# Optimization experiments

Measured on AMD Instinct MI355X. Metric: run time of the kernel, lower is better.

## Reference

```python
import jax, jax.numpy as jnp
import numpy as np

B, N_TOKENS, D, K = 16, 4096, 256, 4096
COMMITMENT_COST = 0.25


def setup_inputs() -> dict:
    key = jax.random.key(0)
    k1, k2 = jax.random.split(key)
    x = jax.random.normal(k1, (B, N_TOKENS, D), dtype=jnp.float32)
    # nn.Embedding init uniform(-1/K, 1/K); scale is irrelevant to correctness,
    # use the same distribution for fidelity.
    codebook = jax.random.uniform(k2, (K, D), dtype=jnp.float32,
                                  minval=-1.0 / K, maxval=1.0 / K)
    return {"x": x, "codebook": codebook}


def reference(x, codebook):
    Bb, Nn, Dd = x.shape
    x_flat = x.reshape(-1, Dd)                                    # [BN, D]
    dist_sq = (jnp.sum(x_flat * x_flat, axis=1, keepdims=True)
               + jnp.sum(codebook * codebook, axis=1)
               - 2.0 * x_flat @ codebook.T)                       # [BN, K]
    dist_sq = jnp.maximum(dist_sq, 0.0)
    idx = jnp.argmin(dist_sq, axis=1)                             # [BN]
    q_flat = codebook[idx]                                        # [BN, D]
    q = q_flat.reshape(x.shape)

    x_sg = jax.lax.stop_gradient(x_flat)
    q_sg = jax.lax.stop_gradient(q_flat)
    codebook_loss = jnp.mean((q_flat - x_sg) ** 2, axis=-1).reshape(Bb, Nn)
    commit_loss = jnp.mean((x_flat - q_sg) ** 2, axis=-1).reshape(Bb, Nn)
    per_token_loss = codebook_loss + COMMITMENT_COST * commit_loss
    mean_vq_loss = jnp.mean(per_token_loss)

    q_st = x + jax.lax.stop_gradient(q - x)                       # straight-through

    counts = jnp.zeros((codebook.shape[0],), dtype=jnp.float32).at[idx].add(1.0)
    avg_probs = counts / x_flat.shape[0]
    perplexity = jnp.exp(-jnp.sum(avg_probs * jnp.log(avg_probs + 1e-10)))

    return q_st, mean_vq_loss, perplexity, idx
```

## Files before the change

### kernel.cpp

```cpp
#include <hip/hip_runtime.h>
#include <hip/hip_bf16.h>
#include <cstdint>
#include <cstddef>

#define D 256
#define NTOK 65536
#define KCODES 4096
#define Q_ELEMS (NTOK * D)
#define DELTA 3.0e-4f
#define CAP 24

typedef short bf16x8 __attribute__((ext_vector_type(8)));
typedef float f32x4 __attribute__((ext_vector_type(4)));
typedef unsigned short ushort8 __attribute__((ext_vector_type(8)));

__device__ __forceinline__ void gload_lds16(const float* g, float* l) {
  __builtin_amdgcn_global_load_lds(
      (const __attribute__((address_space(1))) void*)(g),
      (__attribute__((address_space(3))) void*)(l), 16, 0, 0);
}
__device__ __forceinline__ unsigned short f2bf(float f) {
  __hip_bfloat16 h = __float2bfloat16(f);
  unsigned short u;
  __builtin_memcpy(&u, &h, 2);
  return u;
}

__global__ __launch_bounds__(256) void ee_kernel(const float* __restrict__ cb,
                                                 float* __restrict__ se) {
  const int row = blockIdx.x * 4 + (threadIdx.x >> 6);
  const int lane = threadIdx.x & 63;
  const float4 v = reinterpret_cast<const float4*>(cb + (size_t)row * D)[lane];
  double s = (double)v.x * v.x + (double)v.y * v.y +
             (double)v.z * v.z + (double)v.w * v.w;
#pragma unroll
  for (int o = 32; o > 0; o >>= 1) s += __shfl_down(s, o, 64);
  if (lane == 0) se[row] = (float)s;
}

__global__ __launch_bounds__(256) void xx_kernel(const float* __restrict__ x,
                                                 float* __restrict__ sx) {
  const int row = blockIdx.x * 4 + (threadIdx.x >> 6);
  const int lane = threadIdx.x & 63;
  const float4 v = reinterpret_cast<const float4*>(x + (size_t)row * D)[lane];
  double s = (double)v.x * v.x + (double)v.y * v.y +
             (double)v.z * v.z + (double)v.w * v.w;
#pragma unroll
  for (int o = 32; o > 0; o >>= 1) s += __shfl_down(s, o, 64);
  if (lane == 0) sx[row] = (float)s;
}

__global__ __launch_bounds__(256) void pack_e_kernel(const float* __restrict__ cb,
                                                     unsigned short* __restrict__ bpack) {
  const int gid = blockIdx.x * 256 + threadIdx.x;
  const int c = gid >> 2;
  const int kt = gid & 3;
  const int row = c & 127;
  const int swz = (row & 7) << 3;
  unsigned short* dst = bpack + ((size_t)((c >> 7) * 4 + kt)) * 8192 + row * 64;
  const float* src = cb + (size_t)c * D + kt * 64;
#pragma unroll
  for (int j = 0; j < 8; ++j) {
    ushort8 o;
#pragma unroll
    for (int e = 0; e < 8; ++e) o[e] = f2bf(src[j * 8 + e]);
    *reinterpret_cast<ushort8*>(dst + ((j * 8) ^ swz)) = o;
  }
}

__global__ __launch_bounds__(512, 1) void screen2_kernel(
    const float* __restrict__ x, const unsigned short* __restrict__ bpack,
    const float* __restrict__ se, unsigned int* __restrict__ ccnt_g,
    int* __restrict__ cand_g, float* __restrict__ cval_g,
    float* __restrict__ rm_g) {
  __shared__ __attribute__((aligned(16))) unsigned short bbuf[5][8192];
  __shared__ float se_lds[KCODES];
  __shared__ int cand[256][CAP];
  __shared__ float cval[256][CAP];
  __shared__ unsigned int ccnt[256];

  const int tid = threadIdx.x;
  const int lane = tid & 63;
  const int w = tid >> 6;
  const int l15 = lane & 15;
  const int kg = lane >> 4;
  const int tok0 = blockIdx.x * 256;

  if (tid < 256) ccnt[tid] = 0;
  {
    const float4* s4 = reinterpret_cast<const float4*>(se);
    float4* d4 = reinterpret_cast<float4*>(se_lds);
    d4[tid * 2 + 0] = s4[tid * 2 + 0];
    d4[tid * 2 + 1] = s4[tid * 2 + 1];
  }

  bf16x8 ah[2][8];
#pragma unroll
  for (int gi = 0; gi < 2; ++gi) {
    const int t = tok0 + w * 32 + gi * 16 + l15;
    const float* xp = x + (size_t)t * D;
#pragma unroll
    for (int ks = 0; ks < 8; ++ks) {
      const float4 v0 = *reinterpret_cast<const float4*>(xp + ks * 32 + kg * 8);
      const float4 v1 = *reinterpret_cast<const float4*>(xp + ks * 32 + kg * 8 + 4);
      const float xv[8] = {v0.x, v0.y, v0.z, v0.w, v1.x, v1.y, v1.z, v1.w};
      bf16x8 h;
#pragma unroll
      for (int e = 0; e < 8; ++e) h[e] = (short)f2bf(xv[e]);
      ah[gi][ks] = h;
    }
  }

  auto STAGE = [&](int u) {
    const char* s = (const char*)bpack + (size_t)u * 16384 + w * 2048 + lane * 16;
    char* d = (char*)&bbuf[u % 5][0] + w * 2048;
    gload_lds16((const float*)s, (float*)d);
    gload_lds16((const float*)(s + 1024), (float*)(d + 1024));
  };

  asm volatile("s_waitcnt vmcnt(0)" ::: "memory");
  STAGE(0); STAGE(1); STAGE(2); STAGE(3);
  asm volatile("s_waitcnt vmcnt(6) lgkmcnt(0)" ::: "memory");
  __builtin_amdgcn_s_barrier();
  __builtin_amdgcn_sched_barrier(0);

  float rm[2][4];
#pragma unroll
  for (int fr = 0; fr < 2; ++fr)
#pragma unroll
    for (int q = 0; q < 4; ++q) rm[fr][q] = 3.4e38f;

  f32x4 acc[2][8];

  for (int ct4 = 0; ct4 < 32; ++ct4) {
#pragma unroll
    for (int kt = 0; kt < 4; ++kt) {
      const int u = ct4 * 4 + kt;
      if (u + 4 < 128) STAGE(u + 4);
      if (kt == 0) {
#pragma unroll
        for (int fr = 0; fr < 2; ++fr)
#pragma unroll
          for (int fc = 0; fc < 8; ++fc) acc[fr][fc] = (f32x4){0.f, 0.f, 0.f, 0.f};
      }
      const unsigned short* bb = &bbuf[u % 5][0];
#pragma unroll
      for (int kh = 0; kh < 2; ++kh) {
        const int ks = kt * 2 + kh;
        bf16x8 bfrag[8];
#pragma unroll
        for (int fc = 0; fc < 8; ++fc) {
          const int row = fc * 16 + l15;
          const int off = row * 64 + ((kh * 32 + kg * 8) ^ ((row & 7) << 3));
          bfrag[fc] = *reinterpret_cast<const bf16x8*>(bb + off);
        }
#pragma unroll
        for (int fr = 0; fr < 2; ++fr)
#pragma unroll
          for (int fc = 0; fc < 8; ++fc)
            acc[fr][fc] = __builtin_amdgcn_mfma_f32_16x16x32_bf16(
                ah[fr][ks], bfrag[fc], acc[fr][fc], 0, 0, 0);
      }
      if (kt == 3) {
        float sef[8];
#pragma unroll
        for (int fc = 0; fc < 8; ++fc)
          sef[fc] = se_lds[ct4 * 128 + fc * 16 + l15];
#pragma unroll
        for (int fr = 0; fr < 2; ++fr)
#pragma unroll
          for (int q = 0; q < 4; ++q) {
            float m = fmaf(-2.0f, acc[fr][0][q], sef[0]);
#pragma unroll
            for (int fc = 1; fc < 8; ++fc)
              m = fminf(m, fmaf(-2.0f, acc[fr][fc][q], sef[fc]));
            m = fminf(m, __shfl_xor(m, 1, 64));
            m = fminf(m, __shfl_xor(m, 2, 64));
            m = fminf(m, __shfl_xor(m, 4, 64));
            m = fminf(m, __shfl_xor(m, 8, 64));
            rm[fr][q] = fminf(rm[fr][q], m);
            const float thr = rm[fr][q] + DELTA;
            const int tl = w * 32 + fr * 16 + kg * 4 + q;
#pragma unroll
            for (int fc = 0; fc < 8; ++fc) {
              const float s = fmaf(-2.0f, acc[fr][fc][q], sef[fc]);
              if (s <= thr) {
                const unsigned p = atomicAdd(&ccnt[tl], 1u);
                if (p < CAP) {
                  cand[tl][p] = ct4 * 128 + fc * 16 + l15;
                  cval[tl][p] = s;
                }
              }
            }
          }
      }
      if (u != 127) {
        if (u <= 123) asm volatile("s_waitcnt vmcnt(6)" ::: "memory");
        else          asm volatile("s_waitcnt vmcnt(0)" ::: "memory");
        __builtin_amdgcn_s_barrier();
        __builtin_amdgcn_sched_barrier(0);
      }
    }
  }

  __syncthreads();
  if (tid < 256) ccnt_g[tok0 + tid] = ccnt[tid];
  if (l15 == 0) {
#pragma unroll
    for (int fr = 0; fr < 2; ++fr)
#pragma unroll
      for (int q = 0; q < 4; ++q)
        rm_g[tok0 + w * 32 + fr * 16 + kg * 4 + q] = rm[fr][q];
  }
  for (int j = tid; j < 256 * CAP; j += 512) {
    const int tk = j / CAP;
    const int p = j - tk * CAP;
    cand_g[(size_t)(tok0 + tk) * CAP + p] = cand[tk][p];
    cval_g[(size_t)(tok0 + tk) * CAP + p] = cval[tk][p];
  }
}

__global__ __launch_bounds__(256) void rescore_kernel(
    const float* __restrict__ x, const float* __restrict__ cb,
    const float* __restrict__ se, const float* __restrict__ sx,
    const unsigned int* __restrict__ ccnt_g, const int* __restrict__ cand_g,
    const float* __restrict__ cval_g, const float* __restrict__ rm_g,
    int* __restrict__ idx_i, float* __restrict__ idxf_out,
    unsigned int* __restrict__ ovf_count, int* __restrict__ ovf_list) {
  const int t = blockIdx.x * 256 + threadIdx.x;
  const unsigned n = ccnt_g[t];
  if (n > CAP) {
    const unsigned p = atomicAdd(ovf_count, 1u);
    ovf_list[p] = t;
    return;
  }
  const float thr = rm_g[t] + DELTA;
  const float sxv = sx[t];
  const float4* xp = reinterpret_cast<const float4*>(x + (size_t)t * D);
  float bq = 3.4e38f;
  int bc = 0x7fffffff;
  for (unsigned k = 0; k < n; ++k) {
    if (cval_g[(size_t)t * CAP + k] > thr) continue;
    const int c = cand_g[(size_t)t * CAP + k];
    const float4* cp = reinterpret_cast<const float4*>(cb + (size_t)c * D);
    float acc = 0.0f;
#pragma unroll 8
    for (int d4 = 0; d4 < 64; ++d4) {
      const float4 xv = xp[d4];
      const float4 ev = cp[d4];
      acc = fmaf(xv.x, ev.x, acc);
      acc = fmaf(xv.y, ev.y, acc);
      acc = fmaf(xv.z, ev.z, acc);
      acc = fmaf(xv.w, ev.w, acc);
    }
    const float r = sxv + se[c];
    const float q = r - 2.0f * acc;
    if (q < bq || (q == bq && c < bc)) { bq = q; bc = c; }
  }
  idx_i[t] = bc;
  idxf_out[t] = (float)bc;
}

__global__ __launch_bounds__(256) void ovf_kernel(
    const float* __restrict__ x, const float* __restrict__ cb,
    const float* __restrict__ se, const float* __restrict__ sx,
    const unsigned int* __restrict__ ovf_count, const int* __restrict__ ovf_list,
    int* __restrict__ idx_i, float* __restrict__ idxf_out) {
  __shared__ float bvv[256];
  __shared__ int bii[256];
  const int tid = threadIdx.x;
  const unsigned cnt = *ovf_count;
  for (unsigned i = blockIdx.x; i < cnt; i += gridDim.x) {
    const int t = ovf_list[i];
    const float sxv = sx[t];
    const float4* xp = reinterpret_cast<const float4*>(x + (size_t)t * D);
    float bq = 3.4e38f;
    int bc = 0x7fffffff;
    for (int c = tid; c < KCODES; c += 256) {
      const float4* cp = reinterpret_cast<const float4*>(cb + (size_t)c * D);
      float acc = 0.0f;
#pragma unroll 8
      for (int d4 = 0; d4 < 64; ++d4) {
        const float4 xv = xp[d4];
        const float4 ev = cp[d4];
        acc = fmaf(xv.x, ev.x, acc);
        acc = fmaf(xv.y, ev.y, acc);
        acc = fmaf(xv.z, ev.z, acc);
        acc = fmaf(xv.w, ev.w, acc);
      }
      const float r = sxv + se[c];
      const float q = r - 2.0f * acc;
      if (q < bq || (q == bq && c < bc)) { bq = q; bc = c; }
    }
    bvv[tid] = bq;
    bii[tid] = bc;
    __syncthreads();
    for (int o = 128; o > 0; o >>= 1) {
      if (tid < o) {
        const float v2 = bvv[tid + o];
        const int c2 = bii[tid + o];
        if (v2 < bvv[tid] || (v2 == bvv[tid] && c2 < bii[tid])) {
          bvv[tid] = v2;
          bii[tid] = c2;
        }
      }
      __syncthreads();
    }
    if (tid == 0) {
      idx_i[t] = bii[0];
      idxf_out[t] = (float)bii[0];
    }
    __syncthreads();
  }
}

__global__ __launch_bounds__(256) void argmin_fb_kernel(const float* __restrict__ x,
                                                        const float* __restrict__ cb,
                                                        const float* __restrict__ se,
                                                        const float* __restrict__ sx,
                                                        int* __restrict__ idx_out,
                                                        float* __restrict__ idxf_out) {
  __shared__ __attribute__((aligned(16))) float xs[64 * 128];
  __shared__ __attribute__((aligned(16))) float es[64 * 128];
  const int tid = threadIdx.x;
  const int lane = tid & 63;
  const int w = tid >> 6;
  const int wt = w & 1;
  const int wc = w >> 1;
  const int tgl = lane & 7;
  const int cgl = lane >> 3;
  const int t0 = wt * 64 + tgl * 8;
  const int c0 = wc * 64 + cgl * 8;
  const int tok0 = blockIdx.x * 128;
  float sxf[8];
#pragma unroll
  for (int i = 0; i < 8; ++i) sxf[i] = sx[tok0 + t0 + i];
  float bv[8];
  int bi[8];
#pragma unroll
  for (int i = 0; i < 8; ++i) { bv[i] = 3.4e38f; bi[i] = 0; }
  for (int ct = 0; ct < KCODES / 128; ++ct) {
    float acc[8][8] = {};
    for (int kt = 0; kt < 4; ++kt) {
      __syncthreads();
      {
        const float* xsrc = x + (size_t)tok0 * D + kt * 64;
        const float* esrc = cb + (size_t)(ct * 128) * D + kt * 64;
#pragma unroll
        for (int p = 0; p < 8; ++p) {
          const int idx = p * 256 + tid;
          const int t = idx >> 4;
          const int c = idx & 15;
          const int colp = (t + 8 * (c >> 1)) & 127;
          const float4 xv = *reinterpret_cast<const float4*>(xsrc + (size_t)t * D + c * 4);
          float* xd = &xs[(c * 4) * 128 + colp];
          xd[0] = xv.x; xd[128] = xv.y; xd[256] = xv.z; xd[384] = xv.w;
          const float4 ev = *reinterpret_cast<const float4*>(esrc + (size_t)t * D + c * 4);
          float* ed = &es[(c * 4) * 128 + colp];
          ed[0] = ev.x; ed[128] = ev.y; ed[256] = ev.z; ed[384] = ev.w;
        }
      }
      __syncthreads();
      for (int kp = 0; kp < 8; ++kp) {
        const float* xb = &xs[(kp * 8) * 128 + ((t0 + 8 * kp) & 127)];
        const float* eb = &es[(kp * 8) * 128 + ((c0 + 8 * kp) & 127)];
#pragma unroll
        for (int k2 = 0; k2 < 8; ++k2) {
          const float4 xv0 = *reinterpret_cast<const float4*>(xb + k2 * 128);
          const float4 xv1 = *reinterpret_cast<const float4*>(xb + k2 * 128 + 4);
          const float4 ev0 = *reinterpret_cast<const float4*>(eb + k2 * 128);
          const float4 ev1 = *reinterpret_cast<const float4*>(eb + k2 * 128 + 4);
          const float xa[8] = {xv0.x, xv0.y, xv0.z, xv0.w, xv1.x, xv1.y, xv1.z, xv1.w};
          const float ea[8] = {ev0.x, ev0.y, ev0.z, ev0.w, ev1.x, ev1.y, ev1.z, ev1.w};
#pragma unroll
          for (int i = 0; i < 8; ++i)
#pragma unroll
            for (int j = 0; j < 8; ++j) acc[i][j] = fmaf(xa[i], ea[j], acc[i][j]);
        }
      }
    }
#pragma unroll
    for (int j = 0; j < 8; ++j) {
      const int cidx = ct * 128 + c0 + j;
      const float sef = se[cidx];
#pragma unroll
      for (int i = 0; i < 8; ++i) {
        const float r = sxf[i] + sef;
        const float s = r - 2.0f * acc[i][j];
        if (s < bv[i]) { bv[i] = s; bi[i] = cidx; }
      }
    }
  }
  __syncthreads();
  float* red_val = xs;
  int* red_idx = reinterpret_cast<int*>(xs + 128 * 17);
  const int g = wc * 8 + cgl;
#pragma unroll
  for (int i = 0; i < 8; ++i) {
    red_val[(t0 + i) * 17 + g] = bv[i];
    red_idx[(t0 + i) * 17 + g] = bi[i];
  }
  __syncthreads();
  if (tid < 128) {
    float v = red_val[tid * 17 + 0];
    int ix = red_idx[tid * 17 + 0];
#pragma unroll
    for (int gg = 1; gg < 16; ++gg) {
      const float vv = red_val[tid * 17 + gg];
      const int ii = red_idx[tid * 17 + gg];
      if (vv < v || (vv == v && ii < ix)) { v = vv; ix = ii; }
    }
    idx_out[tok0 + tid] = ix;
    idxf_out[tok0 + tid] = (float)ix;
  }
}

__global__ __launch_bounds__(256) void finalize_kernel(const float* __restrict__ x,
                                                       const float* __restrict__ cb,
                                                       const int* __restrict__ idx,
                                                       float* __restrict__ q_out,
                                                       unsigned int* __restrict__ counts,
                                                       double* __restrict__ partials) {
  __shared__ double tok_s[16];
  const int tid = threadIdx.x;
  const int lt = tid >> 4;
  const int ld = tid & 15;
  const int t = blockIdx.x * 16 + lt;
  const int id = idx[t];
  const float* xp = x + (size_t)t * D + ld * 16;
  const float* ep = cb + (size_t)id * D + ld * 16;
  float* qp = q_out + (size_t)t * D + ld * 16;
  float s = 0.0f;
#pragma unroll
  for (int c = 0; c < 4; ++c) {
    const float4 xv = reinterpret_cast<const float4*>(xp)[c];
    const float4 ev = reinterpret_cast<const float4*>(ep)[c];
    const float d0 = ev.x - xv.x, d1 = ev.y - xv.y;
    const float d2 = ev.z - xv.z, d3 = ev.w - xv.w;
    s = fmaf(d0, d0, s);
    s = fmaf(d1, d1, s);
    s = fmaf(d2, d2, s);
    s = fmaf(d3, d3, s);
    float4 qv;
    qv.x = xv.x + d0;
    qv.y = xv.y + d1;
    qv.z = xv.z + d2;
    qv.w = xv.w + d3;
    reinterpret_cast<float4*>(qp)[c] = qv;
  }
#pragma unroll
  for (int o = 8; o > 0; o >>= 1) s += __shfl_down(s, o, 16);
  if (ld == 0) {
    atomicAdd(&counts[id], 1u);
    tok_s[lt] = (double)s;
  }
  __syncthreads();
  if (tid == 0) {
    double bs = 0.0;
    for (int i = 0; i < 16; ++i) bs += tok_s[i];
    partials[blockIdx.x] = bs;
  }
}

__global__ __launch_bounds__(256) void final_kernel(const unsigned int* __restrict__ counts,
                                                    const double* __restrict__ partials,
                                                    float* __restrict__ loss_out,
                                                    float* __restrict__ perp_out) {
  __shared__ double sh[256];
  const int tid = threadIdx.x;
  double ls = 0.0;
  for (int i = tid; i < NTOK / 16; i += 256) ls += partials[i];
  sh[tid] = ls;
  __syncthreads();
#pragma unroll
  for (int o = 128; o > 0; o >>= 1) {
    if (tid < o) sh[tid] += sh[tid + o];
    __syncthreads();
  }
  if (tid == 0) {
    *loss_out = (float)(sh[0] * (1.25 / (256.0 * 65536.0)));
  }
  __syncthreads();
  double hs = 0.0;
  for (int i = tid; i < KCODES; i += 256) {
    const float p = (float)counts[i] / 65536.0f;
    hs += (double)(p * logf(p + 1e-10f));
  }
  sh[tid] = hs;
  __syncthreads();
#pragma unroll
  for (int o = 128; o > 0; o >>= 1) {
    if (tid < o) sh[tid] += sh[tid + o];
    __syncthreads();
  }
  if (tid == 0) *perp_out = expf((float)(-sh[0]));
}

extern "C" void kernel_launch(void* const* d_in, const int* in_sizes, int n_in,
                              void* d_out, int out_size, void* d_ws, size_t ws_size,
                              hipStream_t stream) {
  (void)in_sizes; (void)n_in; (void)out_size;
  const float* x = (const float*)d_in[0];
  const float* cb = (const float*)d_in[1];

  float* out = (float*)d_out;
  float* q_out = out;
  float* loss_out = out + (size_t)Q_ELEMS;
  float* perp_out = out + (size_t)Q_ELEMS + 1;
  float* idxf_out = out + (size_t)Q_ELEMS + 2;

  char* ws = (char*)d_ws;
  float* se = (float*)(ws + 0);
  unsigned int* counts = (unsigned int*)(ws + (16 << 10));
  double* partials = (double*)(ws + (32 << 10));
  int* idx_i = (int*)(ws + (64 << 10));
  float* sx = (float*)(ws + (320 << 10));
  unsigned int* ovf_count = (unsigned int*)(ws + (576 << 10));
  int* ovf_list = (int*)(ws + (580 << 10));
  unsigned int* ccnt_g = (unsigned int*)(ws + (1 << 20));
  float* rm_g = (float*)(ws + (3 << 19));
  int* cand_g = (int*)(ws + (2 << 20));
  float* cval_g = (float*)(ws + (8 << 20));
  unsigned short* bpack = (unsigned short*)(ws + (14 << 20));

  hipMemsetAsync(counts, 0, KCODES * sizeof(unsigned int), stream);
  hipMemsetAsync(ovf_count, 0, sizeof(unsigned int), stream);
  ee_kernel<<<KCODES / 4, 256, 0, stream>>>(cb, se);
  xx_kernel<<<NTOK / 4, 256, 0, stream>>>(x, sx);

  if (ws_size >= (size_t)20 * 1024 * 1024) {
    pack_e_kernel<<<64, 256, 0, stream>>>(cb, bpack);
    screen2_kernel<<<NTOK / 256, 512, 0, stream>>>(x, bpack, se, ccnt_g, cand_g,
                                                   cval_g, rm_g);
    rescore_kernel<<<NTOK / 256, 256, 0, stream>>>(x, cb, se, sx, ccnt_g, cand_g,
                                                   cval_g, rm_g, idx_i, idxf_out,
                                                   ovf_count, ovf_list);
    ovf_kernel<<<64, 256, 0, stream>>>(x, cb, se, sx, ovf_count, ovf_list,
                                       idx_i, idxf_out);
  } else {
    argmin_fb_kernel<<<NTOK / 128, 256, 0, stream>>>(x, cb, se, sx, idx_i, idxf_out);
  }
  finalize_kernel<<<NTOK / 16, 256, 0, stream>>>(x, cb, idx_i, q_out, counts, partials);
  final_kernel<<<1, 256, 0, stream>>>(counts, partials, loss_out, perp_out);
}
```

Before: 396.5 us.

## Fuse rescore with finalize, pack candidates, shrink screen blocks for two-per-CU occupancy

The screening kernel now uses 256-thread blocks over 128 tokens with a 3-deep LDS ring, so two blocks can share a CU. Codebook norms are held in LDS as bf16, and each candidate's score and index are packed into a single 32-bit word, with the cap lowered to 16. The rescore kernel now also computes ||x||^2, gathers q, writes the straight-through output and accumulates loss and counts, which removes the separate xx and finalize passes over x. Risks: lower-precision candidate scores and norms, more overflow tokens from the smaller cap, and a full barrier after every k-step in place of the previous finer-grained waits.

```diff
diff --git a/kernel.cpp b/kernel.cpp
--- a/kernel.cpp
+++ b/kernel.cpp
@@ -8,7 +8,7 @@
 #define KCODES 4096
 #define Q_ELEMS (NTOK * D)
 #define DELTA 3.0e-4f
-#define CAP 24
+#define CAP 16
 
 typedef short bf16x8 __attribute__((ext_vector_type(8)));
 typedef float f32x4 __attribute__((ext_vector_type(4)));
@@ -24,6 +24,11 @@
   unsigned short u;
   __builtin_memcpy(&u, &h, 2);
   return u;
+}
+__device__ __forceinline__ float bf2f(unsigned short u) {
+  __hip_bfloat16 h;
+  __builtin_memcpy(&h, &u, 2);
+  return __bfloat162float(h);
 }
 
 __global__ __launch_bounds__(256) void ee_kernel(const float* __restrict__ cb,
@@ -68,30 +73,33 @@
   }
 }
 
-__global__ __launch_bounds__(512, 1) void screen2_kernel(
+__global__ __launch_bounds__(256, 2) void screen3_kernel(
     const float* __restrict__ x, const unsigned short* __restrict__ bpack,
     const float* __restrict__ se, unsigned int* __restrict__ ccnt_g,
-    int* __restrict__ cand_g, float* __restrict__ cval_g,
-    float* __restrict__ rm_g) {
-  __shared__ __attribute__((aligned(16))) unsigned short bbuf[5][8192];
-  __shared__ float se_lds[KCODES];
-  __shared__ int cand[256][CAP];
-  __shared__ float cval[256][CAP];
-  __shared__ unsigned int ccnt[256];
+    unsigned int* __restrict__ cand_g, float* __restrict__ rm_g) {
+  __shared__ __attribute__((aligned(16))) unsigned short bbuf[3][8192];
+  __shared__ __attribute__((aligned(16))) unsigned short se_lds[KCODES];
+  __shared__ unsigned int cand[128][CAP];
+  __shared__ unsigned int ccnt[128];
 
   const int tid = threadIdx.x;
   const int lane = tid & 63;
   const int w = tid >> 6;
   const int l15 = lane & 15;
   const int kg = lane >> 4;
-  const int tok0 = blockIdx.x * 256;
-
-  if (tid < 256) ccnt[tid] = 0;
+  const int tok0 = blockIdx.x * 128;
+
+  if (tid < 128) ccnt[tid] = 0;
   {
-    const float4* s4 = reinterpret_cast<const float4*>(se);
-    float4* d4 = reinterpret_cast<float4*>(se_lds);
-    d4[tid * 2 + 0] = s4[tid * 2 + 0];
-    d4[tid * 2 + 1] = s4[tid * 2 + 1];
+    const float4* s4 = reinterpret_cast<const float4*>(se) + tid * 4;
+    const float4 a = s4[0], b = s4[1], c = s4[2], d = s4[3];
+    ushort8 o0, o1;
+    o0[0] = f2bf(a.x); o0[1] = f2bf(a.y); o0[2] = f2bf(a.z); o0[3] = f2bf(a.w);
+    o0[4] = f2bf(b.x); o0[5] = f2bf(b.y); o0[6] = f2bf(b.z); o0[7] = f2bf(b.w);
+    o1[0] = f2bf(c.x); o1[1] = f2bf(c.y); o1[2] = f2bf(c.z); o1[3] = f2bf(c.w);
+    o1[4] = f2bf(d.x); o1[5] = f2bf(d.y); o1[6] = f2bf(d.z); o1[7] = f2bf(d.w);
+    *reinterpret_cast<ushort8*>(&se_lds[tid * 16]) = o0;
+    *reinterpret_cast<ushort8*>(&se_lds[tid * 16 + 8]) = o1;
   }
 
   bf16x8 ah[2][8];
@@ -112,18 +120,14 @@
   }
 
   auto STAGE = [&](int u) {
-    const char* s = (const char*)bpack + (size_t)u * 16384 + w * 2048 + lane * 16;
-    char* d = (char*)&bbuf[u % 5][0] + w * 2048;
+    const char* s = (const char*)bpack + (size_t)u * 16384 + w * 4096 + lane * 16;
+    char* d = (char*)&bbuf[u % 3][0] + w * 4096;
     gload_lds16((const float*)s, (float*)d);
     gload_lds16((const float*)(s + 1024), (float*)(d + 1024));
+    gload_lds16((const float*)(s + 2048), (float*)(d + 2048));
+    gload_lds16((const float*)(s + 3072), (float*)(d + 3072));
   };
 
-  asm volatile("s_waitcnt vmcnt(0)" ::: "memory");
-  STAGE(0); STAGE(1); STAGE(2); STAGE(3);
-  asm volatile("s_waitcnt vmcnt(6) lgkmcnt(0)" ::: "memory");
-  __builtin_amdgcn_s_barrier();
-  __builtin_amdgcn_sched_barrier(0);
-
   float rm[2][4];
 #pragma unroll
   for (int fr = 0; fr < 2; ++fr)
@@ -131,19 +135,23 @@
     for (int q = 0; q < 4; ++q) rm[fr][q] = 3.4e38f;
 
   f32x4 acc[2][8];
+
+  STAGE(0);
+  STAGE(1);
+  __syncthreads();
 
   for (int ct4 = 0; ct4 < 32; ++ct4) {
 #pragma unroll
     for (int kt = 0; kt < 4; ++kt) {
       const int u = ct4 * 4 + kt;
-      if (u + 4 < 128) STAGE(u + 4);
+      if (u + 2 < 128) STAGE(u + 2);
       if (kt == 0) {
 #pragma unroll
         for (int fr = 0; fr < 2; ++fr)
 #pragma unroll
           for (int fc = 0; fc < 8; ++fc) acc[fr][fc] = (f32x4){0.f, 0.f, 0.f, 0.f};
       }
-      const unsigned short* bb = &bbuf[u % 5][0];
+      const unsigned short* bb = &bbuf[u % 3][0];
 #pragma unroll
       for (int kh = 0; kh < 2; ++kh) {
         const int ks = kt * 2 + kh;
@@ -165,7 +173,7 @@
         float sef[8];
 #pragma unroll
         for (int fc = 0; fc < 8; ++fc)
-          sef[fc] = se_lds[ct4 * 128 + fc * 16 + l15];
+          sef[fc] = bf2f(se_lds[ct4 * 128 + fc * 16 + l15]);
 #pragma unroll
         for (int fr = 0; fr < 2; ++fr)
 #pragma unroll
@@ -186,25 +194,18 @@
               const float s = fmaf(-2.0f, acc[fr][fc][q], sef[fc]);
               if (s <= thr) {
                 const unsigned p = atomicAdd(&ccnt[tl], 1u);
-                if (p < CAP) {
-                  cand[tl][p] = ct4 * 128 + fc * 16 + l15;
-                  cval[tl][p] = s;
-                }
+                if (p < CAP)
+                  cand[tl][p] = ((unsigned)f2bf(s) << 16) |
+                                (unsigned)(ct4 * 128 + fc * 16 + l15);
               }
             }
           }
       }
-      if (u != 127) {
-        if (u <= 123) asm volatile("s_waitcnt vmcnt(6)" ::: "memory");
-        else          asm volatile("s_waitcnt vmcnt(0)" ::: "memory");
-        __builtin_amdgcn_s_barrier();
-        __builtin_amdgcn_sched_barrier(0);
-      }
-    }
-  }
-
-  __syncthreads();
-  if (tid < 256) ccnt_g[tok0 + tid] = ccnt[tid];
+      __syncthreads();
+    }
+  }
+
+  if (tid < 128) ccnt_g[tok0 + tid] = ccnt[tid];
   if (l15 == 0) {
 #pragma unroll
     for (int fr = 0; fr < 2; ++fr)
@@ -212,67 +213,132 @@
       for (int q = 0; q < 4; ++q)
         rm_g[tok0 + w * 32 + fr * 16 + kg * 4 + q] = rm[fr][q];
   }
-  for (int j = tid; j < 256 * CAP; j += 512) {
-    const int tk = j / CAP;
-    const int p = j - tk * CAP;
-    cand_g[(size_t)(tok0 + tk) * CAP + p] = cand[tk][p];
-    cval_g[(size_t)(tok0 + tk) * CAP + p] = cval[tk][p];
-  }
-}
-
-__global__ __launch_bounds__(256) void rescore_kernel(
+  for (int j = tid; j < 128 * CAP; j += 256)
+    cand_g[(size_t)tok0 * CAP + j] = cand[j >> 4][j & 15];
+}
+
+__global__ __launch_bounds__(256) void rescore_fused_kernel(
     const float* __restrict__ x, const float* __restrict__ cb,
-    const float* __restrict__ se, const float* __restrict__ sx,
-    const unsigned int* __restrict__ ccnt_g, const int* __restrict__ cand_g,
-    const float* __restrict__ cval_g, const float* __restrict__ rm_g,
-    int* __restrict__ idx_i, float* __restrict__ idxf_out,
-    unsigned int* __restrict__ ovf_count, int* __restrict__ ovf_list) {
-  const int t = blockIdx.x * 256 + threadIdx.x;
+    const float* __restrict__ se, const unsigned int* __restrict__ ccnt_g,
+    const unsigned int* __restrict__ cand_g, const float* __restrict__ rm_g,
+    float* __restrict__ q_out, unsigned int* __restrict__ counts,
+    double* __restrict__ partials, float* __restrict__ idxf_out,
+    int* __restrict__ idx_i, unsigned int* __restrict__ ovf_count,
+    int* __restrict__ ovf_list) {
+  __shared__ int bc_l[256];
+  __shared__ double loss_l[16];
+  const int tid = threadIdx.x;
+  const int t = blockIdx.x * 256 + tid;
   const unsigned n = ccnt_g[t];
+  int bc = -1;
   if (n > CAP) {
     const unsigned p = atomicAdd(ovf_count, 1u);
     ovf_list[p] = t;
-    return;
-  }
-  const float thr = rm_g[t] + DELTA;
-  const float sxv = sx[t];
-  const float4* xp = reinterpret_cast<const float4*>(x + (size_t)t * D);
-  float bq = 3.4e38f;
-  int bc = 0x7fffffff;
-  for (unsigned k = 0; k < n; ++k) {
-    if (cval_g[(size_t)t * CAP + k] > thr) continue;
-    const int c = cand_g[(size_t)t * CAP + k];
-    const float4* cp = reinterpret_cast<const float4*>(cb + (size_t)c * D);
-    float acc = 0.0f;
+  } else {
+    const float4* xp = reinterpret_cast<const float4*>(x + (size_t)t * D);
+    double sxd = 0.0;
+    for (int d4 = 0; d4 < 64; ++d4) {
+      const float4 v = xp[d4];
+      sxd += (double)v.x * v.x + (double)v.y * v.y +
+             (double)v.z * v.z + (double)v.w * v.w;
+    }
+    const float sxv = (float)sxd;
+    const float thr = rm_g[t] + DELTA;
+    float bq = 3.4e38f;
+    int bcl = 0x7fffffff;
+    for (unsigned k = 0; k < n; ++k) {
+      const unsigned pk = cand_g[(size_t)t * CAP + k];
+      if (bf2f((unsigned short)(pk >> 16)) > thr) continue;
+      const int c = (int)(pk & 0xFFFFu);
+      const float4* cp = reinterpret_cast<const float4*>(cb + (size_t)c * D);
+      float acc = 0.0f;
 #pragma unroll 8
-    for (int d4 = 0; d4 < 64; ++d4) {
-      const float4 xv = xp[d4];
-      const float4 ev = cp[d4];
-      acc = fmaf(xv.x, ev.x, acc);
-      acc = fmaf(xv.y, ev.y, acc);
-      acc = fmaf(xv.z, ev.z, acc);
-      acc = fmaf(xv.w, ev.w, acc);
-    }
-    const float r = sxv + se[c];
-    const float q = r - 2.0f * acc;
-    if (q < bq || (q == bq && c < bc)) { bq = q; bc = c; }
-  }
-  idx_i[t] = bc;
-  idxf_out[t] = (float)bc;
-}
-
-__global__ __launch_bounds__(256) void ovf_kernel(
+      for (int d4 = 0; d4 < 64; ++d4) {
+        const float4 xv = xp[d4];
+        const float4 ev = cp[d4];
+        acc = fmaf(xv.x, ev.x, acc);
+        acc = fmaf(xv.y, ev.y, acc);
+        acc = fmaf(xv.z, ev.z, acc);
+        acc = fmaf(xv.w, ev.w, acc);
+      }
+      const float r = sxv + se[c];
+      const float q = r - 2.0f * acc;
+      if (q < bq || (q == bq && c < bcl)) { bq = q; bcl = c; }
+    }
+    bc = bcl;
+    idx_i[t] = bc;
+    idxf_out[t] = (float)bc;
+    atomicAdd(&counts[bc], 1u);
+  }
+  bc_l[tid] = bc;
+  __syncthreads();
+
+  const int lt = tid >> 4;
+  const int ld = tid & 15;
+  double myl = 0.0;
+  for (int tt = 0; tt < 16; ++tt) {
+    const int tk = tt * 16 + lt;
+    const int bcf = bc_l[tk];
+    float s = 0.0f;
+    if (bcf >= 0) {
+      const int tg = blockIdx.x * 256 + tk;
+      const float* xp = x + (size_t)tg * D + ld * 16;
+      const float* ep = cb + (size_t)bcf * D + ld * 16;
+      float* qp = q_out + (size_t)tg * D + ld * 16;
+#pragma unroll
+      for (int c = 0; c < 4; ++c) {
+        const float4 xv = reinterpret_cast<const float4*>(xp)[c];
+        const float4 ev = reinterpret_cast<const float4*>(ep)[c];
+        const float d0 = ev.x - xv.x, d1 = ev.y - xv.y;
+        const float d2 = ev.z - xv.z, d3 = ev.w - xv.w;
+        s = fmaf(d0, d0, s);
+        s = fmaf(d1, d1, s);
+        s = fmaf(d2, d2, s);
+        s = fmaf(d3, d3, s);
+        float4 qv;
+        qv.x = xv.x + d0;
+        qv.y = xv.y + d1;
+        qv.z = xv.z + d2;
+        qv.w = xv.w + d3;
+        reinterpret_cast<float4*>(qp)[c] = qv;
+      }
+    }
+#pragma unroll
+    for (int o = 8; o > 0; o >>= 1) s += __shfl_down(s, o, 16);
+    if (ld == 0) myl += (double)s;
+  }
+  if (ld == 0) loss_l[lt] = myl;
+  __syncthreads();
+  if (tid == 0) {
+    double bs = 0.0;
+    for (int i = 0; i < 16; ++i) bs += loss_l[i];
+    partials[blockIdx.x] = bs;
+  }
+}
+
+__global__ __launch_bounds__(256) void ovf_fused_kernel(
     const float* __restrict__ x, const float* __restrict__ cb,
-    const float* __restrict__ se, const float* __restrict__ sx,
-    const unsigned int* __restrict__ ovf_count, const int* __restrict__ ovf_list,
-    int* __restrict__ idx_i, float* __restrict__ idxf_out) {
+    const float* __restrict__ se, const unsigned int* __restrict__ ovf_count,
+    const int* __restrict__ ovf_list, float* __restrict__ q_out,
+    unsigned int* __restrict__ counts, double* __restrict__ partial_ovf,
+    float* __restrict__ idxf_out, int* __restrict__ idx_i) {
   __shared__ float bvv[256];
   __shared__ int bii[256];
+  __shared__ double sh[256];
+  __shared__ int bc_sh;
   const int tid = threadIdx.x;
   const unsigned cnt = *ovf_count;
   for (unsigned i = blockIdx.x; i < cnt; i += gridDim.x) {
     const int t = ovf_list[i];
-    const float sxv = sx[t];
+    const float xv1 = x[(size_t)t * D + tid];
+    sh[tid] = (double)xv1 * xv1;
+    __syncthreads();
+    for (int o = 128; o > 0; o >>= 1) {
+      if (tid < o) sh[tid] += sh[tid + o];
+      __syncthreads();
+    }
+    const float sxv = (float)sh[0];
+    __syncthreads();
     const float4* xp = reinterpret_cast<const float4*>(x + (size_t)t * D);
     float bq = 3.4e38f;
     int bc = 0x7fffffff;
@@ -307,11 +373,57 @@
       __syncthreads();
     }
     if (tid == 0) {
+      bc_sh = bii[0];
       idx_i[t] = bii[0];
       idxf_out[t] = (float)bii[0];
-    }
-    __syncthreads();
-  }
+      atomicAdd(&counts[bii[0]], 1u);
+    }
+    __syncthreads();
+    const int bcf = bc_sh;
+    const float ev1 = cb[(size_t)bcf * D + tid];
+    const float dd = ev1 - xv1;
+    q_out[(size_t)t * D + tid] = xv1 + dd;
+    sh[tid] = (double)(dd * dd);
+    __syncthreads();
+    for (int o = 128; o > 0; o >>= 1) {
+      if (tid < o) sh[tid] += sh[tid + o];
+      __syncthreads();
+    }
+    if (tid == 0) atomicAdd(partial_ovf, sh[0]);
+    __syncthreads();
+  }
+}
+
+__global__ __launch_bounds__(256) void final2_kernel(
+    const unsigned int* __restrict__ counts, const double* __restrict__ partials,
+    const double* __restrict__ partial_ovf, float* __restrict__ loss_out,
+    float* __restrict__ perp_out) {
+  __shared__ double sh[256];
+  const int tid = threadIdx.x;
+  double ls = partials[tid];
+  if (tid == 0) ls += *partial_ovf;
+  sh[tid] = ls;
+  __syncthreads();
+#pragma unroll
+  for (int o = 128; o > 0; o >>= 1) {
+    if (tid < o) sh[tid] += sh[tid + o];
+    __syncthreads();
+  }
+  if (tid == 0) *loss_out = (float)(sh[0] * (1.25 / (256.0 * 65536.0)));
+  __syncthreads();
+  double hs = 0.0;
+  for (int i = tid; i < KCODES; i += 256) {
+    const float p = (float)counts[i] / 65536.0f;
+    hs += (double)(p * logf(p + 1e-10f));
+  }
+  sh[tid] = hs;
+  __syncthreads();
+#pragma unroll
+  for (int o = 128; o > 0; o >>= 1) {
+    if (tid < o) sh[tid] += sh[tid + o];
+    __syncthreads();
+  }
+  if (tid == 0) *perp_out = expf((float)(-sh[0]));
 }
 
 __global__ __launch_bounds__(256) void argmin_fb_kernel(const float* __restrict__ x,
@@ -477,9 +589,7 @@
     if (tid < o) sh[tid] += sh[tid + o];
     __syncthreads();
   }
-  if (tid == 0) {
-    *loss_out = (float)(sh[0] * (1.25 / (256.0 * 65536.0)));
-  }
+  if (tid == 0) *loss_out = (float)(sh[0] * (1.25 / (256.0 * 65536.0)));
   __syncthreads();
   double hs = 0.0;
   for (int i = tid; i < KCODES; i += 256) {
@@ -513,33 +623,37 @@
   float* se = (float*)(ws + 0);
   unsigned int* counts = (unsigned int*)(ws + (16 << 10));
   double* partials = (double*)(ws + (32 << 10));
-  int* idx_i = (int*)(ws + (64 << 10));
-  float* sx = (float*)(ws + (320 << 10));
-  unsigned int* ovf_count = (unsigned int*)(ws + (576 << 10));
-  int* ovf_list = (int*)(ws + (580 << 10));
+  double* partial_ovf = (double*)(ws + (96 << 10));
+  int* idx_i = (int*)(ws + (128 << 10));
+  float* sx = (float*)(ws + (384 << 10));
+  unsigned int* ovf_count = (unsigned int*)(ws + (640 << 10));
+  int* ovf_list = (int*)(ws + (644 << 10));
   unsigned int* ccnt_g = (unsigned int*)(ws + (1 << 20));
   float* rm_g = (float*)(ws + (3 << 19));
-  int* cand_g = (int*)(ws + (2 << 20));
-  float* cval_g = (float*)(ws + (8 << 20));
+  unsigned int* cand_g = (unsigned int*)(ws + (2 << 20));
   unsigned short* bpack = (unsigned short*)(ws + (14 << 20));
 
   hipMemsetAsync(counts, 0, KCODES * sizeof(unsigned int), stream);
   hipMemsetAsync(ovf_count, 0, sizeof(unsigned int), stream);
+  hipMemsetAsync(partial_ovf, 0, sizeof(double), stream);
   ee_kernel<<<KCODES / 4, 256, 0, stream>>>(cb, se);
-  xx_kernel<<<NTOK / 4, 256, 0, stream>>>(x, sx);
 
   if (ws_size >= (size_t)20 * 1024 * 1024) {
     pack_e_kernel<<<64, 256, 0, stream>>>(cb, bpack);
-    screen2_kernel<<<NTOK / 256, 512, 0, stream>>>(x, bpack, se, ccnt_g, cand_g,
-                                                   cval_g, rm_g);
-    rescore_kernel<<<NTOK / 256, 256, 0, stream>>>(x, cb, se, sx, ccnt_g, cand_g,
-                                                   cval_g, rm_g, idx_i, idxf_out,
-                                                   ovf_count, ovf_list);
-    ovf_kernel<<<64, 256, 0, stream>>>(x, cb, se, sx, ovf_count, ovf_list,
-                                       idx_i, idxf_out);
+    screen3_kernel<<<NTOK / 128, 256, 0, stream>>>(x, bpack, se, ccnt_g, cand_g,
+                                                   rm_g);
+    rescore_fused_kernel<<<NTOK / 256, 256, 0, stream>>>(
+        x, cb, se, ccnt_g, cand_g, rm_g, q_out, counts, partials, idxf_out,
+        idx_i, ovf_count, ovf_list);
+    ovf_fused_kernel<<<64, 256, 0, stream>>>(x, cb, se, ovf_count, ovf_list,
+                                             q_out, counts, partial_ovf,
+                                             idxf_out, idx_i);
+    final2_kernel<<<1, 256, 0, stream>>>(counts, partials, partial_ovf,
+                                         loss_out, perp_out);
   } else {
+    xx_kernel<<<NTOK / 4, 256, 0, stream>>>(x, sx);
     argmin_fb_kernel<<<NTOK / 128, 256, 0, stream>>>(x, cb, se, sx, idx_i, idxf_out);
-  }
-  finalize_kernel<<<NTOK / 16, 256, 0, stream>>>(x, cb, idx_i, q_out, counts, partials);
-  final_kernel<<<1, 256, 0, stream>>>(counts, partials, loss_out, perp_out);
-}
+    finalize_kernel<<<NTOK / 16, 256, 0, stream>>>(x, cb, idx_i, q_out, counts, partials);
+    final_kernel<<<1, 256, 0, stream>>>(counts, partials, loss_out, perp_out);
+  }
+}
```

New measurement: 468.2 us. 1.18x slower.

## Restructure screening kernel into smaller multi-block-per-CU tiles with packed candidates

Applied to the files above, without the earlier changes.

The candidate-screening kernel now uses 256-thread blocks covering 128 tokens, with launch bounds allowing three blocks per CU. It replaces the 5-deep LDS ring with a double buffer and raises wave priority around the MFMA section. Codebook norms are kept in LDS as bf16, and each candidate's index and bf16 score are packed into one 32-bit word, which halves candidate storage and traffic and lowers CAP to 16. The aim is to gain occupancy and cut LDS and global footprint, at the cost of shallower prefetch, a barrier every step, lower-precision screening values, and more overflow tokens falling back to the slow path.

```diff
diff --git a/kernel.cpp b/kernel.cpp
--- a/kernel.cpp
+++ b/kernel.cpp
@@ -8,7 +8,7 @@
 #define KCODES 4096
 #define Q_ELEMS (NTOK * D)
 #define DELTA 3.0e-4f
-#define CAP 24
+#define CAP 16
 
 typedef short bf16x8 __attribute__((ext_vector_type(8)));
 typedef float f32x4 __attribute__((ext_vector_type(4)));
@@ -24,6 +24,11 @@
   unsigned short u;
   __builtin_memcpy(&u, &h, 2);
   return u;
+}
+__device__ __forceinline__ float bf2f(unsigned short u) {
+  __hip_bfloat16 h;
+  __builtin_memcpy(&h, &u, 2);
+  return __bfloat162float(h);
 }
 
 __global__ __launch_bounds__(256) void ee_kernel(const float* __restrict__ cb,
@@ -68,30 +73,33 @@
   }
 }
 
-__global__ __launch_bounds__(512, 1) void screen2_kernel(
+__global__ __launch_bounds__(256, 3) void screen4_kernel(
     const float* __restrict__ x, const unsigned short* __restrict__ bpack,
     const float* __restrict__ se, unsigned int* __restrict__ ccnt_g,
-    int* __restrict__ cand_g, float* __restrict__ cval_g,
-    float* __restrict__ rm_g) {
-  __shared__ __attribute__((aligned(16))) unsigned short bbuf[5][8192];
-  __shared__ float se_lds[KCODES];
-  __shared__ int cand[256][CAP];
-  __shared__ float cval[256][CAP];
-  __shared__ unsigned int ccnt[256];
+    unsigned int* __restrict__ cand_g, float* __restrict__ rm_g) {
+  __shared__ __attribute__((aligned(16))) unsigned short bbuf[2][8192];
+  __shared__ __attribute__((aligned(16))) unsigned short se_lds[KCODES];
+  __shared__ unsigned int cand[128][CAP];
+  __shared__ unsigned int ccnt[128];
 
   const int tid = threadIdx.x;
   const int lane = tid & 63;
   const int w = tid >> 6;
   const int l15 = lane & 15;
   const int kg = lane >> 4;
-  const int tok0 = blockIdx.x * 256;
-
-  if (tid < 256) ccnt[tid] = 0;
+  const int tok0 = blockIdx.x * 128;
+
+  if (tid < 128) ccnt[tid] = 0;
   {
-    const float4* s4 = reinterpret_cast<const float4*>(se);
-    float4* d4 = reinterpret_cast<float4*>(se_lds);
-    d4[tid * 2 + 0] = s4[tid * 2 + 0];
-    d4[tid * 2 + 1] = s4[tid * 2 + 1];
+    const float4* s4 = reinterpret_cast<const float4*>(se) + tid * 4;
+    const float4 a = s4[0], b = s4[1], c = s4[2], d = s4[3];
+    ushort8 o0, o1;
+    o0[0] = f2bf(a.x); o0[1] = f2bf(a.y); o0[2] = f2bf(a.z); o0[3] = f2bf(a.w);
+    o0[4] = f2bf(b.x); o0[5] = f2bf(b.y); o0[6] = f2bf(b.z); o0[7] = f2bf(b.w);
+    o1[0] = f2bf(c.x); o1[1] = f2bf(c.y); o1[2] = f2bf(c.z); o1[3] = f2bf(c.w);
+    o1[4] = f2bf(d.x); o1[5] = f2bf(d.y); o1[6] = f2bf(d.z); o1[7] = f2bf(d.w);
+    *reinterpret_cast<ushort8*>(&se_lds[tid * 16]) = o0;
+    *reinterpret_cast<ushort8*>(&se_lds[tid * 16 + 8]) = o1;
   }
 
   bf16x8 ah[2][8];
@@ -112,18 +120,14 @@
   }
 
   auto STAGE = [&](int u) {
-    const char* s = (const char*)bpack + (size_t)u * 16384 + w * 2048 + lane * 16;
-    char* d = (char*)&bbuf[u % 5][0] + w * 2048;
+    const char* s = (const char*)bpack + (size_t)u * 16384 + w * 4096 + lane * 16;
+    char* d = (char*)&bbuf[u & 1][0] + w * 4096;
     gload_lds16((const float*)s, (float*)d);
     gload_lds16((const float*)(s + 1024), (float*)(d + 1024));
+    gload_lds16((const float*)(s + 2048), (float*)(d + 2048));
+    gload_lds16((const float*)(s + 3072), (float*)(d + 3072));
   };
 
-  asm volatile("s_waitcnt vmcnt(0)" ::: "memory");
-  STAGE(0); STAGE(1); STAGE(2); STAGE(3);
-  asm volatile("s_waitcnt vmcnt(6) lgkmcnt(0)" ::: "memory");
-  __builtin_amdgcn_s_barrier();
-  __builtin_amdgcn_sched_barrier(0);
-
   float rm[2][4];
 #pragma unroll
   for (int fr = 0; fr < 2; ++fr)
@@ -131,19 +135,23 @@
     for (int q = 0; q < 4; ++q) rm[fr][q] = 3.4e38f;
 
   f32x4 acc[2][8];
+
+  STAGE(0);
+  __syncthreads();
 
   for (int ct4 = 0; ct4 < 32; ++ct4) {
 #pragma unroll
     for (int kt = 0; kt < 4; ++kt) {
       const int u = ct4 * 4 + kt;
-      if (u + 4 < 128) STAGE(u + 4);
+      if (u + 1 < 128) STAGE(u + 1);
       if (kt == 0) {
 #pragma unroll
         for (int fr = 0; fr < 2; ++fr)
 #pragma unroll
           for (int fc = 0; fc < 8; ++fc) acc[fr][fc] = (f32x4){0.f, 0.f, 0.f, 0.f};
       }
-      const unsigned short* bb = &bbuf[u % 5][0];
+      const unsigned short* bb = &bbuf[u & 1][0];
+      __builtin_amdgcn_s_setprio(1);
 #pragma unroll
       for (int kh = 0; kh < 2; ++kh) {
         const int ks = kt * 2 + kh;
@@ -161,11 +169,12 @@
             acc[fr][fc] = __builtin_amdgcn_mfma_f32_16x16x32_bf16(
                 ah[fr][ks], bfrag[fc], acc[fr][fc], 0, 0, 0);
       }
+      __builtin_amdgcn_s_setprio(0);
       if (kt == 3) {
         float sef[8];
 #pragma unroll
         for (int fc = 0; fc < 8; ++fc)
-          sef[fc] = se_lds[ct4 * 128 + fc * 16 + l15];
+          sef[fc] = bf2f(se_lds[ct4 * 128 + fc * 16 + l15]);
 #pragma unroll
         for (int fr = 0; fr < 2; ++fr)
 #pragma unroll
@@ -186,25 +195,18 @@
               const float s = fmaf(-2.0f, acc[fr][fc][q], sef[fc]);
               if (s <= thr) {
                 const unsigned p = atomicAdd(&ccnt[tl], 1u);
-                if (p < CAP) {
-                  cand[tl][p] = ct4 * 128 + fc * 16 + l15;
-                  cval[tl][p] = s;
-                }
+                if (p < CAP)
+                  cand[tl][p] = ((unsigned)f2bf(s) << 16) |
+                                (unsigned)(ct4 * 128 + fc * 16 + l15);
               }
             }
           }
       }
-      if (u != 127) {
-        if (u <= 123) asm volatile("s_waitcnt vmcnt(6)" ::: "memory");
-        else          asm volatile("s_waitcnt vmcnt(0)" ::: "memory");
-        __builtin_amdgcn_s_barrier();
-        __builtin_amdgcn_sched_barrier(0);
-      }
-    }
-  }
-
-  __syncthreads();
-  if (tid < 256) ccnt_g[tok0 + tid] = ccnt[tid];
+      __syncthreads();
+    }
+  }
+
+  if (tid < 128) ccnt_g[tok0 + tid] = ccnt[tid];
   if (l15 == 0) {
 #pragma unroll
     for (int fr = 0; fr < 2; ++fr)
@@ -212,21 +214,17 @@
       for (int q = 0; q < 4; ++q)
         rm_g[tok0 + w * 32 + fr * 16 + kg * 4 + q] = rm[fr][q];
   }
-  for (int j = tid; j < 256 * CAP; j += 512) {
-    const int tk = j / CAP;
-    const int p = j - tk * CAP;
-    cand_g[(size_t)(tok0 + tk) * CAP + p] = cand[tk][p];
-    cval_g[(size_t)(tok0 + tk) * CAP + p] = cval[tk][p];
-  }
+  for (int j = tid; j < 128 * CAP; j += 256)
+    cand_g[(size_t)tok0 * CAP + j] = cand[j >> 4][j & 15];
 }
 
 __global__ __launch_bounds__(256) void rescore_kernel(
     const float* __restrict__ x, const float* __restrict__ cb,
     const float* __restrict__ se, const float* __restrict__ sx,
-    const unsigned int* __restrict__ ccnt_g, const int* __restrict__ cand_g,
-    const float* __restrict__ cval_g, const float* __restrict__ rm_g,
-    int* __restrict__ idx_i, float* __restrict__ idxf_out,
-    unsigned int* __restrict__ ovf_count, int* __restrict__ ovf_list) {
+    const unsigned int* __restrict__ ccnt_g, const unsigned int* __restrict__ cand_g,
+    const float* __restrict__ rm_g, int* __restrict__ idx_i,
+    float* __restrict__ idxf_out, unsigned int* __restrict__ ovf_count,
+    int* __restrict__ ovf_list) {
   const int t = blockIdx.x * 256 + threadIdx.x;
   const unsigned n = ccnt_g[t];
   if (n > CAP) {
@@ -240,8 +238,9 @@
   float bq = 3.4e38f;
   int bc = 0x7fffffff;
   for (unsigned k = 0; k < n; ++k) {
-    if (cval_g[(size_t)t * CAP + k] > thr) continue;
-    const int c = cand_g[(size_t)t * CAP + k];
+    const unsigned pk = cand_g[(size_t)t * CAP + k];
+    if (bf2f((unsigned short)(pk >> 16)) > thr) continue;
+    const int c = (int)(pk & 0xFFFFu);
     const float4* cp = reinterpret_cast<const float4*>(cb + (size_t)c * D);
     float acc = 0.0f;
 #pragma unroll 8
@@ -477,9 +476,7 @@
     if (tid < o) sh[tid] += sh[tid + o];
     __syncthreads();
   }
-  if (tid == 0) {
-    *loss_out = (float)(sh[0] * (1.25 / (256.0 * 65536.0)));
-  }
+  if (tid == 0) *loss_out = (float)(sh[0] * (1.25 / (256.0 * 65536.0)));
   __syncthreads();
   double hs = 0.0;
   for (int i = tid; i < KCODES; i += 256) {
@@ -513,14 +510,13 @@
   float* se = (float*)(ws + 0);
   unsigned int* counts = (unsigned int*)(ws + (16 << 10));
   double* partials = (double*)(ws + (32 << 10));
-  int* idx_i = (int*)(ws + (64 << 10));
-  float* sx = (float*)(ws + (320 << 10));
-  unsigned int* ovf_count = (unsigned int*)(ws + (576 << 10));
-  int* ovf_list = (int*)(ws + (580 << 10));
+  int* idx_i = (int*)(ws + (128 << 10));
+  float* sx = (float*)(ws + (384 << 10));
+  unsigned int* ovf_count = (unsigned int*)(ws + (640 << 10));
+  int* ovf_list = (int*)(ws + (644 << 10));
   unsigned int* ccnt_g = (unsigned int*)(ws + (1 << 20));
   float* rm_g = (float*)(ws + (3 << 19));
-  int* cand_g = (int*)(ws + (2 << 20));
-  float* cval_g = (float*)(ws + (8 << 20));
+  unsigned int* cand_g = (unsigned int*)(ws + (2 << 20));
   unsigned short* bpack = (unsigned short*)(ws + (14 << 20));
 
   hipMemsetAsync(counts, 0, KCODES * sizeof(unsigned int), stream);
@@ -530,10 +526,10 @@
 
   if (ws_size >= (size_t)20 * 1024 * 1024) {
     pack_e_kernel<<<64, 256, 0, stream>>>(cb, bpack);
-    screen2_kernel<<<NTOK / 256, 512, 0, stream>>>(x, bpack, se, ccnt_g, cand_g,
-                                                   cval_g, rm_g);
+    screen4_kernel<<<NTOK / 128, 256, 0, stream>>>(x, bpack, se, ccnt_g, cand_g,
+                                                   rm_g);
     rescore_kernel<<<NTOK / 256, 256, 0, stream>>>(x, cb, se, sx, ccnt_g, cand_g,
-                                                   cval_g, rm_g, idx_i, idxf_out,
+                                                   rm_g, idx_i, idxf_out,
                                                    ovf_count, ovf_list);
     ovf_kernel<<<64, 256, 0, stream>>>(x, cb, se, sx, ovf_count, ovf_list,
                                        idx_i, idxf_out);
```

Measured after the change: 525.9 us. 32.7% more time.
